# Optimization experiments

Hardware: AMD Instinct MI355X
Metric: run time of the kernel (lower is better)

Reference implementation:

```python
import jax, jax.numpy as jnp
import numpy as np

D_MODEL = 1024
N_HEADS = 16
D_K = D_MODEL // N_HEADS
EPS = 1e-6


def setup_inputs() -> dict:
    key = jax.random.key(0)
    ks = jax.random.split(key, 9)
    s = 1.0 / np.sqrt(D_MODEL)
    x = jax.random.normal(ks[0], (4, 4096, D_MODEL), dtype=jnp.float32)
    Wq = jax.random.uniform(ks[1], (D_MODEL, D_MODEL), jnp.float32, -s, s)
    bq = jax.random.uniform(ks[2], (D_MODEL,), jnp.float32, -s, s)
    Wk = jax.random.uniform(ks[3], (D_MODEL, D_MODEL), jnp.float32, -s, s)
    bk = jax.random.uniform(ks[4], (D_MODEL,), jnp.float32, -s, s)
    Wv = jax.random.uniform(ks[5], (D_MODEL, D_MODEL), jnp.float32, -s, s)
    bv = jax.random.uniform(ks[6], (D_MODEL,), jnp.float32, -s, s)
    Wo = jax.random.uniform(ks[7], (D_MODEL, D_MODEL), jnp.float32, -s, s)
    bo = jax.random.uniform(ks[8], (D_MODEL,), jnp.float32, -s, s)
    return {"x": x, "Wq": Wq, "bq": bq, "Wk": Wk, "bk": bk,
            "Wv": Wv, "bv": bv, "Wo": Wo, "bo": bo}


def _feature_map(t):
    # elu(x) + 1
    return jax.nn.elu(t) + 1.0


def reference(x, Wq, bq, Wk, bk, Wv, bv, Wo, bo):
    b, s, _ = x.shape
    # projections, split into heads: [b, h, s, d_k]
    def heads(t):
        return t.reshape(b, s, N_HEADS, D_K).transpose(0, 2, 1, 3)
    q = _feature_map(heads(x @ Wq + bq))
    k = _feature_map(heads(x @ Wk + bk))
    v = heads(x @ Wv + bv)
    # kv accumulation: [b, h, d_k, d_k]
    kv = jnp.einsum('bhsd,bhse->bhde', k, v)
    # normalizer: q . sum_s k  -> [b, h, s, 1]
    z = jnp.einsum('bhsd,bhd->bhs', q, k.sum(axis=2))[..., None]
    out = jnp.einsum('bhsd,bhde->bhse', q, kv) / (z + EPS)
    out = out.transpose(0, 2, 1, 3).reshape(b, s, D_MODEL)
    return out @ Wo + bo
```

## Files before the change

kernel.cpp:

```cpp
#include <hip/hip_runtime.h>


typedef __bf16 bf16;
typedef float  f32x4  __attribute__((ext_vector_type(4)));
typedef short  s16x8  __attribute__((ext_vector_type(8)));
typedef bf16   bf16x4 __attribute__((ext_vector_type(4)));

#define BATCH 4
#define SEQ   4096
#define DM    1024
#define NH    16
#define DK    64
#define MROWS (BATCH*SEQ)
#define EPSV  1e-6f

__device__ __forceinline__ void async_cp16(const bf16* g, bf16* l) {
  __builtin_amdgcn_global_load_lds((const __attribute__((address_space(1))) void*)g,
                                   (__attribute__((address_space(3))) void*)l,
                                   16, 0, 0);
}

__global__ __launch_bounds__(256) void conv_x_kernel(const float* __restrict__ x,
                                                     bf16* __restrict__ xb) {
  int i = (blockIdx.x * 256 + threadIdx.x) * 4;
  float4 f = *reinterpret_cast<const float4*>(x + i);
  bf16x4 o;
  o[0] = (bf16)f.x; o[1] = (bf16)f.y; o[2] = (bf16)f.z; o[3] = (bf16)f.w;
  *reinterpret_cast<bf16x4*>(xb + i) = o;
}

__global__ __launch_bounds__(256) void conv_w_kernel(const float* __restrict__ W0,
                                                     const float* __restrict__ W1,
                                                     const float* __restrict__ W2,
                                                     const float* __restrict__ W3,
                                                     bf16* __restrict__ Wt) {
  __shared__ bf16 tt[64][72];
  const int z = blockIdx.z;
  const float* W = (z == 0) ? W0 : (z == 1) ? W1 : (z == 2) ? W2 : W3;
  const int n0 = blockIdx.x * 64, k0 = blockIdx.y * 64;
  const int tid = threadIdx.x;
#pragma unroll
  for (int i = 0; i < 4; ++i) {
    const int c = tid + i * 256;
    const int krow = c >> 4, nch = c & 15;
    float4 f = *reinterpret_cast<const float4*>(W + (size_t)(k0 + krow) * DM + n0 + nch * 4);
    tt[nch * 4 + 0][krow] = (bf16)f.x;
    tt[nch * 4 + 1][krow] = (bf16)f.y;
    tt[nch * 4 + 2][krow] = (bf16)f.z;
    tt[nch * 4 + 3][krow] = (bf16)f.w;
  }
  __syncthreads();
#pragma unroll
  for (int i = 0; i < 2; ++i) {
    const int c = tid + i * 256;
    const int nrow = c >> 3, kch = c & 7;
    *reinterpret_cast<uint4*>(Wt + (size_t)(z * DM + n0 + nrow) * DM + k0 + kch * 8) =
        *reinterpret_cast<const uint4*>(&tt[nrow][kch * 8]);
  }
}

template <int MODE>
__global__ __launch_bounds__(512, 2) void gemm_bf16(const bf16* __restrict__ A,
                                                    const bf16* __restrict__ Bt,
                                                    void* __restrict__ Cout, int ldc,
                                                    const float* __restrict__ b0,
                                                    const float* __restrict__ b1,
                                                    const float* __restrict__ b2,
                                                    bf16* __restrict__ kt,
                                                    bf16* __restrict__ vt) {
  constexpr int K  = 1024;
  constexpr int BK = 64;
  constexpr int NT = K / BK;
  __shared__ __align__(16) char smem[131072];

  const int tid  = threadIdx.x;
  const int wv   = tid >> 6, lane = tid & 63;
  const int quad = lane >> 4, l16 = lane & 15;
  const int swk  = l16 & 7;

  const int w = blockIdx.y * gridDim.x + blockIdx.x;
  const int j = w >> 3;
  const int bm0 = (((w & 7) << 3) + (j & 7)) << 8;
  const int bn0 = (j >> 3) << 8;

  const int wm = wv >> 2;
  const int wn = wv & 3;

  f32x4 acc[8][4] = {};
  s16x8 af[4][2];
  s16x8 bq[2][2][2];

  const int srow = wv * 8 + (lane >> 3);
  const int scol = ((lane & 7) ^ (lane >> 3)) * 8;
  const bf16* Ag = A  + (size_t)(bm0 + srow) * K + scol;
  const bf16* Bg = Bt + (size_t)(bn0 + srow) * K + scol;
  const int sbase = wv * 1024;

#define STAGE_A(t_, h_) do {                                                   \
    const bf16* g_ = Ag + (size_t)((h_) * 128) * K + (t_) * BK;                \
    char* l_ = smem + ((t_) & 1) * 32768 + (h_) * 16384 + sbase;               \
    async_cp16(g_, (bf16*)l_);                                                 \
    async_cp16(g_ + (size_t)64 * K, (bf16*)(l_ + 8192));                       \
  } while (0)
#define STAGE_B(t_, h_) do {                                                   \
    const bf16* g_ = Bg + (size_t)((h_) * 128) * K + (t_) * BK;                \
    char* l_ = smem + 65536 + ((t_) & 1) * 32768 + (h_) * 16384 + sbase;       \
    async_cp16(g_, (bf16*)l_);                                                 \
    async_cp16(g_ + (size_t)64 * K, (bf16*)(l_ + 8192));                       \
  } while (0)
#define LDA(pb_, qm_) do {                                                     \
    const char* ab_ = smem + (pb_) * 32768 +                                   \
        (size_t)(wm * 128 + (qm_) * 64 + l16) * 128;                           \
    _Pragma("unroll") for (int mi = 0; mi < 4; ++mi)                           \
      _Pragma("unroll") for (int ks = 0; ks < 2; ++ks)                         \
        af[mi][ks] = *reinterpret_cast<const s16x8*>(                          \
            ab_ + mi * 2048 + (((ks * 4 + quad) ^ swk) << 4));                 \
  } while (0)
#define LDB(pb_, qn_) do {                                                     \
    const char* bb_ = smem + 65536 + (pb_) * 32768 +                           \
        (size_t)(wn * 64 + (qn_) * 32 + l16) * 128;                            \
    _Pragma("unroll") for (int ni = 0; ni < 2; ++ni)                           \
      _Pragma("unroll") for (int ks = 0; ks < 2; ++ks)                         \
        bq[qn_][ni][ks] = *reinterpret_cast<const s16x8*>(                     \
            bb_ + ni * 2048 + (((ks * 4 + quad) ^ swk) << 4));                 \
  } while (0)
#define MFMA_Q(qm_, qn_) do {                                                  \
    _Pragma("unroll") for (int mi = 0; mi < 4; ++mi)                           \
      _Pragma("unroll") for (int ni = 0; ni < 2; ++ni)                         \
        _Pragma("unroll") for (int ks = 0; ks < 2; ++ks)                       \
          acc[(qm_) * 4 + mi][(qn_) * 2 + ni] =                                \
              __builtin_amdgcn_mfma_f32_16x16x32_bf16(                         \
                  af[mi][ks], bq[qn_][ni][ks],                                 \
                  acc[(qm_) * 4 + mi][(qn_) * 2 + ni], 0, 0, 0);               \
  } while (0)

  STAGE_B(0, 0); STAGE_A(0, 0); STAGE_B(0, 1); STAGE_A(0, 1);
  STAGE_B(1, 0); STAGE_A(1, 0);
  asm volatile("s_waitcnt vmcnt(4)");
  __builtin_amdgcn_s_barrier();
  __builtin_amdgcn_sched_barrier(0);
  LDA(0, 0); LDB(0, 0); LDB(0, 1);
  __builtin_amdgcn_sched_barrier(0);

#pragma unroll 2
  for (int t = 0; t < NT; ++t) {
    const int p = t & 1;
    if (t + 1 < NT) STAGE_B(t + 1, 1);
    asm volatile("s_waitcnt lgkmcnt(0)");
    __builtin_amdgcn_sched_barrier(0);
    __builtin_amdgcn_s_setprio(1);
    MFMA_Q(0, 0); MFMA_Q(0, 1);
    __builtin_amdgcn_s_setprio(0);
    LDA(p, 1);
    __builtin_amdgcn_sched_barrier(0);
    if (t + 1 < NT) STAGE_A(t + 1, 1);
    asm volatile("s_waitcnt lgkmcnt(0)");
    __builtin_amdgcn_sched_barrier(0);
    __builtin_amdgcn_s_setprio(1);
    MFMA_Q(1, 0); MFMA_Q(1, 1);
    __builtin_amdgcn_s_setprio(0);
    __builtin_amdgcn_s_barrier();
    __builtin_amdgcn_sched_barrier(0);
    if (t + 2 < NT) { STAGE_B(t + 2, 0); STAGE_A(t + 2, 0); }
    if (t + 1 < NT) {
      if (t + 2 < NT) asm volatile("s_waitcnt vmcnt(4)");
      else            asm volatile("s_waitcnt vmcnt(0)");
      __builtin_amdgcn_s_barrier();
      __builtin_amdgcn_sched_barrier(0);
      LDA(p ^ 1, 0); LDB(p ^ 1, 0); LDB(p ^ 1, 1);
      __builtin_amdgcn_sched_barrier(0);
    }
  }

  if (MODE == 0) {
    const int part = bn0 >> 10;
    if (part == 0) {
      bf16* C = (bf16*)Cout;
      bf16 (*Cw)[64] = (bf16(*)[64])(smem + wv * 16384);
#pragma unroll
      for (int ni = 0; ni < 4; ++ni) {
        const int n_l = ni * 16 + l16;
        const float bias = b0[bn0 + wn * 64 + n_l];
#pragma unroll
        for (int mi = 0; mi < 8; ++mi)
#pragma unroll
          for (int r = 0; r < 4; ++r) {
            float v = acc[mi][ni][r] + bias;
            v = (v > 0.f) ? (v + 1.f) : __expf(v);
            const int row = mi * 16 + quad * 4 + r;
            Cw[row][n_l ^ ((row & 7) << 3)] = (bf16)v;
          }
      }
#pragma unroll
      for (int i = 0; i < 16; ++i) {
        const int row = i * 8 + (lane >> 3), ch = lane & 7;
        *reinterpret_cast<uint4*>(C + (size_t)(bm0 + wm * 128 + row) * ldc +
                                  bn0 + wn * 64 + ch * 8) =
            *reinterpret_cast<const uint4*>(&Cw[row][(ch ^ (row & 7)) * 8]);
      }
    } else {
      bf16* T = (part == 1) ? kt : vt;
      const float* bp = (part == 1) ? b1 : b2;
      const int b  = bm0 >> 12;
      const int h  = ((bn0 & 1023) >> 6) + wn;
      const int s_loc = (bm0 & 4095) + wm * 128;
      bf16* base = T + (size_t)(b * 16 + h) * 64 * 4096 + s_loc;
      char* sl = smem + wv * 16384;
#pragma unroll
      for (int ni = 0; ni < 4; ++ni) {
        const int d = ni * 16 + l16;
        const float bias = bp[(bn0 + wn * 64 + d) & 1023];
#pragma unroll
        for (int mi = 0; mi < 8; ++mi) {
          bf16x4 o;
#pragma unroll
          for (int r = 0; r < 4; ++r) {
            float v = acc[mi][ni][r] + bias;
            if (part == 1) v = (v > 0.f) ? (v + 1.f) : __expf(v);
            o[r] = (bf16)v;
          }
          const int sb = mi * 32 + quad * 8;
          *reinterpret_cast<uint2*>(sl + d * 256 + (sb ^ ((d & 7) << 4))) =
              *reinterpret_cast<const uint2*>(&o);
        }
      }
#pragma unroll
      for (int i = 0; i < 16; ++i) {
        const int d = i * 4 + (lane >> 4), ch = l16;
        const uint4 val = *reinterpret_cast<const uint4*>(
            sl + d * 256 + ((ch * 16) ^ ((d & 7) << 4)));
        *reinterpret_cast<uint4*>(base + (size_t)d * 4096 + ch * 8) = val;
      }
    }
  } else {
    float* C = (float*)Cout;
    float (*Cwf)[64] = (float(*)[64])(smem + wv * 16384);
#pragma unroll
    for (int h = 0; h < 2; ++h) {
#pragma unroll
      for (int ni = 0; ni < 4; ++ni) {
        const int n_l = ni * 16 + l16;
        const float bias = b0[bn0 + wn * 64 + n_l];
#pragma unroll
        for (int mi = 0; mi < 4; ++mi)
#pragma unroll
          for (int r = 0; r < 4; ++r) {
            const int row = mi * 16 + quad * 4 + r;
            Cwf[row][n_l ^ ((row & 7) << 2)] = acc[h * 4 + mi][ni][r] + bias;
          }
      }
#pragma unroll
      for (int i = 0; i < 16; ++i) {
        const int row = i * 4 + (lane >> 4), ch = lane & 15;
        *reinterpret_cast<float4*>(C + (size_t)(bm0 + wm * 128 + h * 64 + row) * ldc +
                                   bn0 + wn * 64 + ch * 4) =
            *reinterpret_cast<const float4*>(&Cwf[row][(ch ^ (row & 7)) * 4]);
      }
    }
  }
#undef STAGE_A
#undef STAGE_B
#undef LDA
#undef LDB
#undef MFMA_Q
}

__global__ __launch_bounds__(256) void kvk_mfma_kernel(const bf16* __restrict__ KT,
                                                       const bf16* __restrict__ VT,
                                                       float* __restrict__ kvT,
                                                       float* __restrict__ ksum) {
  __shared__ bf16 Ks[64][136];
  __shared__ bf16 Vs[64][136];
  const int bh = blockIdx.y;
  const int tid = threadIdx.x;
  const int wv = tid >> 6, lane = tid & 63;
  const int quad = lane >> 4, l16 = lane & 15;
  const size_t tb = (size_t)bh * 64 * 4096;
  const int s0b = blockIdx.x * 512;

  f32x4 acc[4][4] = {};
  float ksp[4] = {};

  for (int cc = 0; cc < 4; ++cc) {
    const int s0 = s0b + cc * 128;
    __syncthreads();
#pragma unroll
    for (int i = 0; i < 4; ++i) {
      const int c = tid + i * 256;
      const int row = c >> 4, ch = c & 15;
      const size_t go = tb + (size_t)row * 4096 + s0 + ch * 8;
      uint4 kk = *reinterpret_cast<const uint4*>(KT + go);
      *reinterpret_cast<uint4*>(&Ks[row][ch * 8]) = kk;
      *reinterpret_cast<uint4*>(&Vs[row][ch * 8]) =
          *reinterpret_cast<const uint4*>(VT + go);
      const bf16* kp = reinterpret_cast<const bf16*>(&kk);
      float t = 0.f;
#pragma unroll
      for (int jj = 0; jj < 8; ++jj) t += (float)kp[jj];
      ksp[i] += t;
    }
    __syncthreads();
    const int kb = wv * 32 + quad * 8;
    s16x8 vfr[4], kfr[4];
#pragma unroll
    for (int mi = 0; mi < 4; ++mi) {
      vfr[mi] = *reinterpret_cast<const s16x8*>(&Vs[mi * 16 + l16][kb]);
      kfr[mi] = *reinterpret_cast<const s16x8*>(&Ks[mi * 16 + l16][kb]);
    }
#pragma unroll
    for (int mi = 0; mi < 4; ++mi)
#pragma unroll
      for (int ni = 0; ni < 4; ++ni)
        acc[mi][ni] = __builtin_amdgcn_mfma_f32_16x16x32_bf16(vfr[mi], kfr[ni],
                                                              acc[mi][ni], 0, 0, 0);
  }
#pragma unroll
  for (int mi = 0; mi < 4; ++mi)
#pragma unroll
    for (int ni = 0; ni < 4; ++ni)
#pragma unroll
      for (int r = 0; r < 4; ++r) {
        const int e = mi * 16 + quad * 4 + r;
        const int d = ni * 16 + l16;
        atomicAdd(&kvT[(size_t)bh * 4096 + e * 64 + d], acc[mi][ni][r]);
      }
#pragma unroll
  for (int i = 0; i < 4; ++i)
#pragma unroll
    for (int o = 8; o > 0; o >>= 1)
      ksp[i] += __shfl_down(ksp[i], o, 16);
  if (l16 == 0) {
    const int g = tid >> 4;
#pragma unroll
    for (int i = 0; i < 4; ++i)
      atomicAdd(&ksum[bh * 64 + g + 16 * i], ksp[i]);
  }
}

__global__ __launch_bounds__(256) void attn_kernel(const bf16* __restrict__ Qb,
                                                   const float* __restrict__ kvT,
                                                   const float* __restrict__ ksum,
                                                   bf16* __restrict__ ATT) {
  __shared__ bf16 qs[128][72];
  __shared__ bf16 kvs[64][72];
  __shared__ bf16 Ps[128][72];
  __shared__ float zr[128];
  __shared__ float kss[64];
  const int bh = blockIdx.y;
  const int b = bh >> 4, h = bh & 15;
  const int s0 = blockIdx.x * 128;
  const int tid = threadIdx.x, wave = tid >> 6, lane = tid & 63;
  const int quad = lane >> 4, l16 = lane & 15;
  const size_t base = (size_t)b * SEQ * DM;
  const int colQ = h * 64;

#pragma unroll
  for (int i = 0; i < 4; ++i) {
    const int c = tid + i * 256;
    const int row = c >> 3, off = (c & 7) * 8;
    *reinterpret_cast<uint4*>(&qs[row][off]) =
        *reinterpret_cast<const uint4*>(Qb + base + (size_t)(s0 + row) * DM + colQ + off);
  }
  const float* kvg = kvT + (size_t)bh * 4096;
#pragma unroll
  for (int i = 0; i < 4; ++i) {
    const int c = tid + i * 256;
    const int row = c >> 4, off = (c & 15) * 4;
    float4 f = *reinterpret_cast<const float4*>(kvg + row * 64 + off);
    bf16x4 o;
    o[0] = (bf16)f.x; o[1] = (bf16)f.y; o[2] = (bf16)f.z; o[3] = (bf16)f.w;
    *reinterpret_cast<bf16x4*>(&kvs[row][off]) = o;
  }
  if (tid < 64) kss[tid] = ksum[bh * 64 + tid];
  __syncthreads();

  if (tid < 128) {
    float z = 0.f;
#pragma unroll
    for (int d = 0; d < 64; d += 4) {
      bf16x4 q4 = *reinterpret_cast<const bf16x4*>(&qs[tid][d]);
      z += (float)q4[0] * kss[d] + (float)q4[1] * kss[d + 1] +
           (float)q4[2] * kss[d + 2] + (float)q4[3] * kss[d + 3];
    }
    zr[tid] = 1.0f / (z + EPSV);
  }
  __syncthreads();

  const int wn = wave * 32;
  f32x4 pacc[4][2] = {};
#pragma unroll
  for (int ks = 0; ks < 2; ++ks) {
    s16x8 af[4], bf2[2];
#pragma unroll
    for (int mi = 0; mi < 4; ++mi)
      af[mi] = *reinterpret_cast<const s16x8*>(&kvs[mi * 16 + l16][ks * 32 + quad * 8]);
#pragma unroll
    for (int ni = 0; ni < 2; ++ni)
      bf2[ni] = *reinterpret_cast<const s16x8*>(&qs[wn + ni * 16 + l16][ks * 32 + quad * 8]);
#pragma unroll
    for (int mi = 0; mi < 4; ++mi)
#pragma unroll
      for (int ni = 0; ni < 2; ++ni)
        pacc[mi][ni] = __builtin_amdgcn_mfma_f32_16x16x32_bf16(af[mi], bf2[ni],
                                                               pacc[mi][ni], 0, 0, 0);
  }
#pragma unroll
  for (int ni = 0; ni < 2; ++ni) {
    const int s = wn + ni * 16 + l16;
    const float zi = zr[s];
#pragma unroll
    for (int mi = 0; mi < 4; ++mi) {
      bf16x4 o;
#pragma unroll
      for (int r = 0; r < 4; ++r) o[r] = (bf16)(pacc[mi][ni][r] * zi);
      *reinterpret_cast<bf16x4*>(&Ps[s][mi * 16 + quad * 4]) = o;
    }
  }
  __syncthreads();
#pragma unroll
  for (int i = 0; i < 4; ++i) {
    const int c = tid + i * 256;
    const int row = c >> 3, ch = c & 7;
    *reinterpret_cast<uint4*>(ATT + ((size_t)b * SEQ + s0 + row) * DM + h * 64 + ch * 8) =
        *reinterpret_cast<const uint4*>(&Ps[row][ch * 8]);
  }
}

extern "C" void kernel_launch(void* const* d_in, const int* in_sizes, int n_in,
                              void* d_out, int out_size, void* d_ws, size_t ws_size,
                              hipStream_t stream) {
  const float* x  = (const float*)d_in[0];
  const float* Wq = (const float*)d_in[1];
  const float* bq = (const float*)d_in[2];
  const float* Wk = (const float*)d_in[3];
  const float* bk = (const float*)d_in[4];
  const float* Wv = (const float*)d_in[5];
  const float* bv = (const float*)d_in[6];
  const float* Wo = (const float*)d_in[7];
  const float* bo = (const float*)d_in[8];
  float* out = (float*)d_out;

  char* ws = (char*)d_ws;
  bf16*  Xb   = (bf16*)ws;   ws += (size_t)MROWS * DM * 2;
  bf16*  Wt   = (bf16*)ws;   ws += (size_t)4 * DM * DM * 2;
  bf16*  Qb   = (bf16*)ws;   ws += (size_t)MROWS * DM * 2;
  bf16*  KT   = (bf16*)ws;   ws += (size_t)64 * 64 * 4096 * 2;
  bf16*  VT   = (bf16*)ws;   ws += (size_t)64 * 64 * 4096 * 2;
  bf16*  ATT  = (bf16*)ws;   ws += (size_t)MROWS * DM * 2;
  float* kvT  = (float*)ws;  ws += (size_t)64 * 4096 * 4;
  float* ksum = (float*)ws;  ws += (size_t)64 * 64 * 4;

  (void)hipMemsetAsync(kvT, 0, (size_t)64 * 4096 * 4 + (size_t)64 * 64 * 4, stream);

  conv_x_kernel<<<MROWS * DM / 1024, 256, 0, stream>>>(x, Xb);
  conv_w_kernel<<<dim3(16, 16, 4), 256, 0, stream>>>(Wq, Wk, Wv, Wo, Wt);
  gemm_bf16<0><<<dim3(12, 64), 512, 0, stream>>>(Xb, Wt, Qb, DM, bq, bk, bv, KT, VT);
  kvk_mfma_kernel<<<dim3(8, 64), 256, 0, stream>>>(KT, VT, kvT, ksum);
  attn_kernel<<<dim3(32, 64), 256, 0, stream>>>(Qb, kvT, ksum, ATT);
  gemm_bf16<1><<<dim3(4, 64), 512, 0, stream>>>(ATT, Wt + (size_t)3 * DM * DM, out, DM,
                                                bo, bo, bo, nullptr, nullptr);
}
```

Baseline: 342.5 us.

## Fuse conversion kernels and reduce kv atomics via LDS cross-wave reduction

Merges the x and weight bf16 conversion kernels into one launch, using a flat block index to pick the path. In the kv accumulation kernel, each block now covers twice the sequence span, halving the grid. The four waves' partial kv tiles are summed through a 64KB LDS buffer before global atomicAdd, replacing per-wave atomics. The extra LDS shrinks occupancy and the grid is smaller, which trades parallelism for far fewer atomics.

```diff
diff --git a/kernel.cpp b/kernel.cpp
--- a/kernel.cpp
+++ b/kernel.cpp
@@ -13,6 +13,7 @@
 #define DK    64
 #define MROWS (BATCH*SEQ)
 #define EPSV  1e-6f
+#define NXB   (MROWS*DM/1024)
 
 __device__ __forceinline__ void async_cp16(const bf16* g, bf16* l) {
   __builtin_amdgcn_global_load_lds((const __attribute__((address_space(1))) void*)g,
@@ -20,25 +21,28 @@
                                    16, 0, 0);
 }
 
-__global__ __launch_bounds__(256) void conv_x_kernel(const float* __restrict__ x,
-                                                     bf16* __restrict__ xb) {
-  int i = (blockIdx.x * 256 + threadIdx.x) * 4;
-  float4 f = *reinterpret_cast<const float4*>(x + i);
-  bf16x4 o;
-  o[0] = (bf16)f.x; o[1] = (bf16)f.y; o[2] = (bf16)f.z; o[3] = (bf16)f.w;
-  *reinterpret_cast<bf16x4*>(xb + i) = o;
-}
-
-__global__ __launch_bounds__(256) void conv_w_kernel(const float* __restrict__ W0,
-                                                     const float* __restrict__ W1,
-                                                     const float* __restrict__ W2,
-                                                     const float* __restrict__ W3,
-                                                     bf16* __restrict__ Wt) {
+__global__ __launch_bounds__(256) void conv_fused_kernel(const float* __restrict__ x,
+                                                         bf16* __restrict__ xb,
+                                                         const float* __restrict__ W0,
+                                                         const float* __restrict__ W1,
+                                                         const float* __restrict__ W2,
+                                                         const float* __restrict__ W3,
+                                                         bf16* __restrict__ Wt) {
   __shared__ bf16 tt[64][72];
-  const int z = blockIdx.z;
+  const int bid = blockIdx.x;
+  const int tid = threadIdx.x;
+  if (bid < NXB) {
+    int i = (bid * 256 + tid) * 4;
+    float4 f = *reinterpret_cast<const float4*>(x + i);
+    bf16x4 o;
+    o[0] = (bf16)f.x; o[1] = (bf16)f.y; o[2] = (bf16)f.z; o[3] = (bf16)f.w;
+    *reinterpret_cast<bf16x4*>(xb + i) = o;
+    return;
+  }
+  const int b2 = bid - NXB;
+  const int z = b2 >> 8;
   const float* W = (z == 0) ? W0 : (z == 1) ? W1 : (z == 2) ? W2 : W3;
-  const int n0 = blockIdx.x * 64, k0 = blockIdx.y * 64;
-  const int tid = threadIdx.x;
+  const int n0 = (b2 & 15) * 64, k0 = ((b2 >> 4) & 15) * 64;
 #pragma unroll
   for (int i = 0; i < 4; ++i) {
     const int c = tid + i * 256;
@@ -271,17 +275,18 @@
                                                        float* __restrict__ ksum) {
   __shared__ bf16 Ks[64][136];
   __shared__ bf16 Vs[64][136];
+  __shared__ float red[4][4096];
   const int bh = blockIdx.y;
   const int tid = threadIdx.x;
   const int wv = tid >> 6, lane = tid & 63;
   const int quad = lane >> 4, l16 = lane & 15;
   const size_t tb = (size_t)bh * 64 * 4096;
-  const int s0b = blockIdx.x * 512;
+  const int s0b = blockIdx.x * 1024;
 
   f32x4 acc[4][4] = {};
   float ksp[4] = {};
 
-  for (int cc = 0; cc < 4; ++cc) {
+  for (int cc = 0; cc < 8; ++cc) {
     const int s0 = s0b + cc * 128;
     __syncthreads();
 #pragma unroll
@@ -319,11 +324,21 @@
 #pragma unroll
     for (int ni = 0; ni < 4; ++ni)
 #pragma unroll
-      for (int r = 0; r < 4; ++r) {
-        const int e = mi * 16 + quad * 4 + r;
-        const int d = ni * 16 + l16;
-        atomicAdd(&kvT[(size_t)bh * 4096 + e * 64 + d], acc[mi][ni][r]);
-      }
+      for (int r = 0; r < 4; ++r)
+        red[wv][(mi * 16 + quad * 4 + r) * 64 + ni * 16 + l16] = acc[mi][ni][r];
+  __syncthreads();
+#pragma unroll
+  for (int jj = 0; jj < 4; ++jj) {
+    const int c0 = tid * 16 + jj * 4;
+    const float4 s0 = *reinterpret_cast<const float4*>(&red[0][c0]);
+    const float4 s1 = *reinterpret_cast<const float4*>(&red[1][c0]);
+    const float4 s2 = *reinterpret_cast<const float4*>(&red[2][c0]);
+    const float4 s3 = *reinterpret_cast<const float4*>(&red[3][c0]);
+    atomicAdd(&kvT[tb / 64 + c0 + 0], s0.x + s1.x + s2.x + s3.x);
+    atomicAdd(&kvT[tb / 64 + c0 + 1], s0.y + s1.y + s2.y + s3.y);
+    atomicAdd(&kvT[tb / 64 + c0 + 2], s0.z + s1.z + s2.z + s3.z);
+    atomicAdd(&kvT[tb / 64 + c0 + 3], s0.w + s1.w + s2.w + s3.w);
+  }
 #pragma unroll
   for (int i = 0; i < 4; ++i)
 #pragma unroll
@@ -452,10 +467,9 @@
 
   (void)hipMemsetAsync(kvT, 0, (size_t)64 * 4096 * 4 + (size_t)64 * 64 * 4, stream);
 
-  conv_x_kernel<<<MROWS * DM / 1024, 256, 0, stream>>>(x, Xb);
-  conv_w_kernel<<<dim3(16, 16, 4), 256, 0, stream>>>(Wq, Wk, Wv, Wo, Wt);
+  conv_fused_kernel<<<NXB + 1024, 256, 0, stream>>>(x, Xb, Wq, Wk, Wv, Wo, Wt);
   gemm_bf16<0><<<dim3(12, 64), 512, 0, stream>>>(Xb, Wt, Qb, DM, bq, bk, bv, KT, VT);
-  kvk_mfma_kernel<<<dim3(8, 64), 256, 0, stream>>>(KT, VT, kvT, ksum);
+  kvk_mfma_kernel<<<dim3(4, 64), 256, 0, stream>>>(KT, VT, kvT, ksum);
   attn_kernel<<<dim3(32, 64), 256, 0, stream>>>(Qb, kvT, ksum, ATT);
   gemm_bf16<1><<<dim3(4, 64), 512, 0, stream>>>(ATT, Wt + (size_t)3 * DM * DM, out, DM,
                                                 bo, bo, bo, nullptr, nullptr);
```

Result: no change. 349.3 us (+2.0%).
